# Optimization experiments

Hardware: AMD Instinct MI355X
Metric: run time of the kernel (lower is better)

## Reference

```python
import jax, jax.numpy as jnp
import numpy as np

E = 400000   # n_entity
R = 500      # n_relation
D = 128      # embed_dim
B = 2048     # batch of queries
K = 128      # sample_limit (refer neighbors per query)
GAMMA = 24.0
EPS = 2.0


def _xavier(key, fan_out, fan_in):
    lim = np.sqrt(6.0 / (fan_in + fan_out)).astype(np.float32)
    return jax.random.uniform(key, (fan_out, fan_in), minval=-lim, maxval=lim, dtype=jnp.float32)


def setup_inputs() -> dict:
    key = jax.random.key(0)
    ks = jax.random.split(key, 9)
    erange = (GAMMA + EPS) / D
    # tables with the appended zero padding row (as in forward's torch.cat)
    ent = jax.random.uniform(ks[0], (E + R + 1, D), minval=-erange, maxval=erange, dtype=jnp.float32)
    entity_embedding = jnp.concatenate([ent, jnp.zeros((1, D), jnp.float32)], axis=0)
    rel = jax.random.uniform(ks[1], (R + 1, D), minval=-erange, maxval=erange, dtype=jnp.float32)
    relation_embedding = jnp.concatenate([rel, jnp.zeros((1, D), jnp.float32)], axis=0)
    off = jax.random.uniform(ks[2], (R + 1, D), minval=0.0, maxval=erange, dtype=jnp.float32)
    offset_embedding = jnp.concatenate([off, jnp.zeros((1, D), jnp.float32)], axis=0)
    # ProjectionAggregating attention MLP params
    W1 = _xavier(ks[3], D, 2 * D)
    b1 = jnp.zeros((D,), jnp.float32)
    W2 = _xavier(ks[4], D, D)
    b2 = jnp.zeros((D,), jnp.float32)
    anchors = jax.random.randint(ks[5], (B,), 0, E)
    rel_0 = jax.random.randint(ks[6], (B,), 0, R)
    p1_target = jax.random.randint(ks[7], (B, K), 0, E)
    p1_rel = jax.random.randint(ks[8], (B, K), 0, R)
    return {
        'entity_embedding': entity_embedding,
        'relation_embedding': relation_embedding,
        'offset_embedding': offset_embedding,
        'W1': W1, 'b1': b1, 'W2': W2, 'b2': b2,
        'anchors': anchors, 'rel_0': rel_0,
        'p1_target': p1_target, 'p1_rel': p1_rel,
    }


def reference(entity_embedding, relation_embedding, offset_embedding,
              W1, b1, W2, b2, anchors, rel_0, p1_target, p1_rel):
    # ---- '1p' query path of IDN_Q2B_24.forward ----
    h_a = entity_embedding[anchors]            # [B, D]
    r_q = relation_embedding[rel_0]            # [B, D]
    query_emb = h_a + r_q                      # [B, D]
    offset_emb = offset_embedding[rel_0]       # [B, D]  (activation = Identity)
    h_t = entity_embedding[p1_target]          # [B, K, D]  refer_embs
    r_t = relation_embedding[p1_rel]           # [B, K, D]  refer_r
    # ProjectionAggregating (aggr='bias'): bias = refer - (start + refer_r)
    bias = h_t - (h_a[:, None, :] + r_t)       # [B, K, D]
    x = jnp.concatenate([r_t, jnp.broadcast_to(r_q[:, None, :], r_t.shape)], axis=-1)  # [B,K,2D]
    a1 = jax.nn.relu(jnp.einsum('bkf,df->bkd', x, W1) + b1)   # [B, K, D]
    attn = jnp.einsum('bkd,ed->bke', a1, W2) + b2             # [B, K, D]
    final_refer = jnp.sum(attn * bias, axis=-2)               # [B, D]
    final_query = query_emb + final_refer
    return final_query, offset_emb
```

## Files before the change

kernel.cpp:

```cpp
#include <hip/hip_runtime.h>

typedef __attribute__((ext_vector_type(8))) short short8;
typedef __attribute__((ext_vector_type(4))) float f32x4;

#define NRELROWS 502
#define NB 2048
#define DD 128
#define OUT_HALF (NB * DD)

__device__ __forceinline__ short f2bf(float x) {
    union { float f; unsigned u; } c; c.f = x;
    return (short)((c.u + 0x7FFFu + ((c.u >> 16) & 1u)) >> 16);
}

__global__ __launch_bounds__(256) void precompute_kernel(
    const float* __restrict__ rel, const float* __restrict__ W1,
    const float* __restrict__ b1, const float* __restrict__ W2,
    float* __restrict__ U, float* __restrict__ V,
    unsigned short* __restrict__ W2f)
{
    const int bid = blockIdx.x;
    const int tid = threadIdx.x;
    if (bid < 126) {
        __shared__ float srel[4][DD];
        const int r0 = bid << 2;
        for (int i = tid; i < 512; i += 256) {
            const int r = i >> 7, c = i & 127;
            const int rr = r0 + r;
            srel[r][c] = (rr < NRELROWS) ? rel[rr * DD + c] : 0.f;
        }
        __syncthreads();
        const int half = tid >> 7;
        const int d = tid & 127;
        const float* wrow = W1 + d * 256 + half * 128;
        float a0 = 0.f, a1 = 0.f, a2 = 0.f, a3 = 0.f;
#pragma unroll 8
        for (int f = 0; f < 128; f += 4) {
            const float4 wv = *(const float4*)(wrow + f);
            a0 += srel[0][f]*wv.x + srel[0][f+1]*wv.y + srel[0][f+2]*wv.z + srel[0][f+3]*wv.w;
            a1 += srel[1][f]*wv.x + srel[1][f+1]*wv.y + srel[1][f+2]*wv.z + srel[1][f+3]*wv.w;
            a2 += srel[2][f]*wv.x + srel[2][f+1]*wv.y + srel[2][f+2]*wv.z + srel[2][f+3]*wv.w;
            a3 += srel[3][f]*wv.x + srel[3][f+1]*wv.y + srel[3][f+2]*wv.z + srel[3][f+3]*wv.w;
        }
        float res[4] = {a0, a1, a2, a3};
        const float bb = half ? b1[d] : 0.f;
#pragma unroll
        for (int r = 0; r < 4; ++r) {
            if (r0 + r < NRELROWS) {
                if (half) V[(r0 + r) * DD + d] = res[r] + bb;
                else      U[(r0 + r) * DD + d] = res[r];
            }
        }
    } else {
        const int tile = bid - 126;
        const int kt = tile >> 3, nt = tile & 7;
#pragma unroll
        for (int e = 0; e < 2; ++e) {
            const int within = tid * 2 + e;
            const int l = within >> 3, i = within & 7;
            const int n = nt * 16 + (l & 15);
            const int f = kt * 32 + (l >> 4) * 8 + i;
            W2f[tile * 512 + within] = (unsigned short)f2bf(W2[n * 128 + f]);
        }
    }
}

__global__ __launch_bounds__(512, 4) void main_kernel(
    const float* __restrict__ ent, const float* __restrict__ rel,
    const float* __restrict__ off, const float* __restrict__ b2,
    const int* __restrict__ anchors, const int* __restrict__ rel0,
    const int* __restrict__ p1t, const int* __restrict__ p1r,
    const float* __restrict__ U, const float* __restrict__ V,
    const unsigned short* __restrict__ W2f, float* __restrict__ out)
{
    __shared__ float ht[128][DD];
    const int b = blockIdx.x;
    const int tid = threadIdx.x;
    const int w = tid >> 6;
    const int l = tid & 63;
    const int lg = l >> 4;
    const int l15 = l & 15;
    const int half = l >> 5;

    const int aidx = anchors[b];
    const int r0 = rel0[b];
    const int* p1t_b = p1t + (b << 7);
    const int* p1r_b = p1r + (b << 7);

    int rowi[8];
#pragma unroll
    for (int j = 0; j < 8; ++j)
        rowi[j] = p1t_b[(w << 4) + (j << 1) + half];
#pragma unroll
    for (int j = 0; j < 8; ++j) {
        const float* g = ent + (size_t)rowi[j] * DD + ((l & 31) << 2);
        float* lp = &ht[(w << 4) + (j << 1)][0];
        __builtin_amdgcn_global_load_lds(
            (const __attribute__((address_space(1))) unsigned int*)g,
            (__attribute__((address_space(3))) unsigned int*)lp, 16, 0, 0);
    }

    const int relA = p1r_b[(w << 4) + l15];

    f32x4 acc[8];
#pragma unroll
    for (int n = 0; n < 8; ++n) acc[n] = (f32x4)0.f;

    const float* Vrow = V + r0 * DD;
    const float* Urow0 = U + relA * DD;

#pragma unroll
    for (int kt = 0; kt < 4; ++kt) {
        const int f0 = kt * 32 + lg * 8;
        const float4 vv0 = *(const float4*)(Vrow + f0);
        const float4 vv1 = *(const float4*)(Vrow + f0 + 4);
        const float4 u0 = *(const float4*)(Urow0 + f0);
        const float4 u1 = *(const float4*)(Urow0 + f0 + 4);
        short8 af;
        af[0] = f2bf(fmaxf(u0.x + vv0.x, 0.f));
        af[1] = f2bf(fmaxf(u0.y + vv0.y, 0.f));
        af[2] = f2bf(fmaxf(u0.z + vv0.z, 0.f));
        af[3] = f2bf(fmaxf(u0.w + vv0.w, 0.f));
        af[4] = f2bf(fmaxf(u1.x + vv1.x, 0.f));
        af[5] = f2bf(fmaxf(u1.y + vv1.y, 0.f));
        af[6] = f2bf(fmaxf(u1.z + vv1.z, 0.f));
        af[7] = f2bf(fmaxf(u1.w + vv1.w, 0.f));
        const unsigned short* Wk = W2f + (kt << 3) * 512 + (l << 3);
#pragma unroll
        for (int nt = 0; nt < 8; ++nt) {
            const short8 bf = *(const short8*)(Wk + (nt << 9));
            acc[nt] = __builtin_amdgcn_mfma_f32_16x16x32_bf16(af, bf, acc[nt], 0, 0, 0);
        }
    }

    const int4 r4 = *(const int4*)(p1r_b + (w << 4) + (lg << 2));
    const int rr4[4] = {r4.x, r4.y, r4.z, r4.w};
    const float* arow = ent + (size_t)aidx * DD;

    asm volatile("s_waitcnt vmcnt(0)" ::: "memory");
    __builtin_amdgcn_sched_barrier(0);

    float ps[8];
#pragma unroll
    for (int nt = 0; nt < 8; ++nt) ps[nt] = 0.f;
#pragma unroll
    for (int nt = 0; nt < 8; ++nt) {
        const int d = (nt << 4) + l15;
        const float had = arow[d];
        const float b2d = b2[d];
#pragma unroll
        for (int r2 = 0; r2 < 4; ++r2) {
            const float at = acc[nt][r2] + b2d;
            const float hv = ht[(w << 4) + (lg << 2) + r2][d];
            const float rv = rel[rr4[r2] * DD + d];
            ps[nt] += at * (hv - had - rv);
        }
        ps[nt] += __shfl_xor(ps[nt], 16);
        ps[nt] += __shfl_xor(ps[nt], 32);
    }

    __syncthreads();
    float* red = &ht[0][0];
    if (lg == 0) {
#pragma unroll
        for (int nt = 0; nt < 8; ++nt)
            red[w * DD + (nt << 4) + l15] = ps[nt];
    }
    __syncthreads();
    if (tid < DD) {
        const int d = tid;
        float s = 0.f;
#pragma unroll
        for (int ww = 0; ww < 8; ++ww) s += red[ww * DD + d];
        out[(b << 7) + d] = arow[d] + rel[r0 * DD + d] + s;
        out[OUT_HALF + (b << 7) + d] = off[r0 * DD + d];
    }
}

extern "C" void kernel_launch(void* const* d_in, const int* in_sizes, int n_in,
                              void* d_out, int out_size, void* d_ws, size_t ws_size,
                              hipStream_t stream) {
    const float* ent  = (const float*)d_in[0];
    const float* rel  = (const float*)d_in[1];
    const float* off  = (const float*)d_in[2];
    const float* W1   = (const float*)d_in[3];
    const float* b1   = (const float*)d_in[4];
    const float* W2   = (const float*)d_in[5];
    const float* b2   = (const float*)d_in[6];
    const int* anchors = (const int*)d_in[7];
    const int* rel0    = (const int*)d_in[8];
    const int* p1t     = (const int*)d_in[9];
    const int* p1r     = (const int*)d_in[10];
    float* out = (float*)d_out;

    float* U = (float*)d_ws;
    float* V = U + NRELROWS * DD;
    unsigned short* W2f = (unsigned short*)(V + NRELROWS * DD);

    precompute_kernel<<<126 + 32, 256, 0, stream>>>(rel, W1, b1, W2, U, V, W2f);
    main_kernel<<<NB, 512, 0, stream>>>(ent, rel, off, b2, anchors, rel0,
                                        p1t, p1r, U, V, W2f, out);
}
```

Baseline: 61.10 us.

## Process eight queries per block with register-staged gather prefetch and LDS-resident W2

Each block now handles eight queries instead of one, looping over them. The bf16 W2 fragments are built once per block in LDS rather than by a separate precompute pass. The next query's entity rows are prefetched into registers while the current query's MFMA and reduction run, replacing the per-query async global-to-LDS load. This amortizes setup and overlaps the gather latency with compute, but it cuts the grid to 256 blocks and needs more LDS and registers per block, which may lower occupancy and parallelism.

Measured after the change: 66.94 us. 1.1x slower.

```diff
diff --git a/kernel.cpp b/kernel.cpp
--- a/kernel.cpp
+++ b/kernel.cpp
@@ -2,10 +2,13 @@
 
 typedef __attribute__((ext_vector_type(8))) short short8;
 typedef __attribute__((ext_vector_type(4))) float f32x4;
+typedef __attribute__((ext_vector_type(2))) float f32x2;
 
 #define NRELROWS 502
 #define NB 2048
 #define DD 128
+#define QPB 8
+#define NBLK (NB / QPB)
 #define OUT_HALF (NB * DD)
 
 __device__ __forceinline__ short f2bf(float x) {
@@ -15,165 +18,210 @@
 
 __global__ __launch_bounds__(256) void precompute_kernel(
     const float* __restrict__ rel, const float* __restrict__ W1,
-    const float* __restrict__ b1, const float* __restrict__ W2,
-    float* __restrict__ U, float* __restrict__ V,
-    unsigned short* __restrict__ W2f)
+    const float* __restrict__ b1,
+    float* __restrict__ U, float* __restrict__ V)
 {
     const int bid = blockIdx.x;
     const int tid = threadIdx.x;
-    if (bid < 126) {
-        __shared__ float srel[4][DD];
-        const int r0 = bid << 2;
-        for (int i = tid; i < 512; i += 256) {
-            const int r = i >> 7, c = i & 127;
-            const int rr = r0 + r;
-            srel[r][c] = (rr < NRELROWS) ? rel[rr * DD + c] : 0.f;
-        }
-        __syncthreads();
-        const int half = tid >> 7;
-        const int d = tid & 127;
-        const float* wrow = W1 + d * 256 + half * 128;
-        float a0 = 0.f, a1 = 0.f, a2 = 0.f, a3 = 0.f;
+    __shared__ float srel[4][DD];
+    const int r0 = bid << 2;
+    for (int i = tid; i < 512; i += 256) {
+        const int r = i >> 7, c = i & 127;
+        const int rr = r0 + r;
+        srel[r][c] = (rr < NRELROWS) ? rel[rr * DD + c] : 0.f;
+    }
+    __syncthreads();
+    const int half = tid >> 7;
+    const int d = tid & 127;
+    const float* wrow = W1 + d * 256 + half * 128;
+    float a0 = 0.f, a1 = 0.f, a2 = 0.f, a3 = 0.f;
 #pragma unroll 8
-        for (int f = 0; f < 128; f += 4) {
-            const float4 wv = *(const float4*)(wrow + f);
-            a0 += srel[0][f]*wv.x + srel[0][f+1]*wv.y + srel[0][f+2]*wv.z + srel[0][f+3]*wv.w;
-            a1 += srel[1][f]*wv.x + srel[1][f+1]*wv.y + srel[1][f+2]*wv.z + srel[1][f+3]*wv.w;
-            a2 += srel[2][f]*wv.x + srel[2][f+1]*wv.y + srel[2][f+2]*wv.z + srel[2][f+3]*wv.w;
-            a3 += srel[3][f]*wv.x + srel[3][f+1]*wv.y + srel[3][f+2]*wv.z + srel[3][f+3]*wv.w;
-        }
-        float res[4] = {a0, a1, a2, a3};
-        const float bb = half ? b1[d] : 0.f;
-#pragma unroll
-        for (int r = 0; r < 4; ++r) {
-            if (r0 + r < NRELROWS) {
-                if (half) V[(r0 + r) * DD + d] = res[r] + bb;
-                else      U[(r0 + r) * DD + d] = res[r];
-            }
-        }
-    } else {
-        const int tile = bid - 126;
-        const int kt = tile >> 3, nt = tile & 7;
-#pragma unroll
-        for (int e = 0; e < 2; ++e) {
-            const int within = tid * 2 + e;
-            const int l = within >> 3, i = within & 7;
-            const int n = nt * 16 + (l & 15);
-            const int f = kt * 32 + (l >> 4) * 8 + i;
-            W2f[tile * 512 + within] = (unsigned short)f2bf(W2[n * 128 + f]);
-        }
-    }
-}
-
-__global__ __launch_bounds__(512, 4) void main_kernel(
+    for (int f = 0; f < 128; f += 4) {
+        const float4 wv = *(const float4*)(wrow + f);
+        a0 += srel[0][f]*wv.x + srel[0][f+1]*wv.y + srel[0][f+2]*wv.z + srel[0][f+3]*wv.w;
+        a1 += srel[1][f]*wv.x + srel[1][f+1]*wv.y + srel[1][f+2]*wv.z + srel[1][f+3]*wv.w;
+        a2 += srel[2][f]*wv.x + srel[2][f+1]*wv.y + srel[2][f+2]*wv.z + srel[2][f+3]*wv.w;
+        a3 += srel[3][f]*wv.x + srel[3][f+1]*wv.y + srel[3][f+2]*wv.z + srel[3][f+3]*wv.w;
+    }
+    float res[4] = {a0, a1, a2, a3};
+    const float bb = half ? b1[d] : 0.f;
+#pragma unroll
+    for (int r = 0; r < 4; ++r) {
+        if (r0 + r < NRELROWS) {
+            if (half) V[(r0 + r) * DD + d] = res[r] + bb;
+            else      U[(r0 + r) * DD + d] = res[r];
+        }
+    }
+}
+
+__global__ __launch_bounds__(512) void main_kernel(
     const float* __restrict__ ent, const float* __restrict__ rel,
     const float* __restrict__ off, const float* __restrict__ b2,
+    const float* __restrict__ W2,
     const int* __restrict__ anchors, const int* __restrict__ rel0,
     const int* __restrict__ p1t, const int* __restrict__ p1r,
     const float* __restrict__ U, const float* __restrict__ V,
-    const unsigned short* __restrict__ W2f, float* __restrict__ out)
+    float* __restrict__ out)
 {
-    __shared__ float ht[128][DD];
-    const int b = blockIdx.x;
+    extern __shared__ float lds[];
+    float* ht = lds;
+    unsigned short* w2l = (unsigned short*)(lds + DD*DD);
+    float* red = (float*)(w2l + 32 * 512);
+
     const int tid = threadIdx.x;
     const int w = tid >> 6;
     const int l = tid & 63;
     const int lg = l >> 4;
     const int l15 = l & 15;
-    const int half = l >> 5;
-
-    const int aidx = anchors[b];
-    const int r0 = rel0[b];
-    const int* p1t_b = p1t + (b << 7);
-    const int* p1r_b = p1r + (b << 7);
-
-    int rowi[8];
-#pragma unroll
-    for (int j = 0; j < 8; ++j)
-        rowi[j] = p1t_b[(w << 4) + (j << 1) + half];
-#pragma unroll
-    for (int j = 0; j < 8; ++j) {
-        const float* g = ent + (size_t)rowi[j] * DD + ((l & 31) << 2);
-        float* lp = &ht[(w << 4) + (j << 1)][0];
-        __builtin_amdgcn_global_load_lds(
-            (const __attribute__((address_space(1))) unsigned int*)g,
-            (__attribute__((address_space(3))) unsigned int*)lp, 16, 0, 0);
-    }
-
-    const int relA = p1r_b[(w << 4) + l15];
-
-    f32x4 acc[8];
-#pragma unroll
-    for (int n = 0; n < 8; ++n) acc[n] = (f32x4)0.f;
-
-    const float* Vrow = V + r0 * DD;
-    const float* Urow0 = U + relA * DD;
-
-#pragma unroll
-    for (int kt = 0; kt < 4; ++kt) {
-        const int f0 = kt * 32 + lg * 8;
-        const float4 vv0 = *(const float4*)(Vrow + f0);
-        const float4 vv1 = *(const float4*)(Vrow + f0 + 4);
-        const float4 u0 = *(const float4*)(Urow0 + f0);
-        const float4 u1 = *(const float4*)(Urow0 + f0 + 4);
-        short8 af;
-        af[0] = f2bf(fmaxf(u0.x + vv0.x, 0.f));
-        af[1] = f2bf(fmaxf(u0.y + vv0.y, 0.f));
-        af[2] = f2bf(fmaxf(u0.z + vv0.z, 0.f));
-        af[3] = f2bf(fmaxf(u0.w + vv0.w, 0.f));
-        af[4] = f2bf(fmaxf(u1.x + vv1.x, 0.f));
-        af[5] = f2bf(fmaxf(u1.y + vv1.y, 0.f));
-        af[6] = f2bf(fmaxf(u1.z + vv1.z, 0.f));
-        af[7] = f2bf(fmaxf(u1.w + vv1.w, 0.f));
-        const unsigned short* Wk = W2f + (kt << 3) * 512 + (l << 3);
+    const int bq0 = blockIdx.x * QPB;
+
+    for (int i = tid; i < 32 * 512; i += 512) {
+        const int tile = i >> 9, within = i & 511;
+        const int kt = tile >> 3, nt = tile & 7;
+        const int ll = within >> 3, ii = within & 7;
+        const int n = nt * 16 + (ll & 15);
+        const int f = kt * 32 + (ll >> 4) * 8 + ii;
+        w2l[i] = (unsigned short)f2bf(W2[n * 128 + f]);
+    }
+    float b2v[8];
+#pragma unroll
+    for (int nt = 0; nt < 8; ++nt) b2v[nt] = b2[(nt << 4) + l15];
+
+    const int* p1t_0 = p1t + (bq0 << 7);
+    const int* p1r_0 = p1r + (bq0 << 7);
+    int relA = p1r_0[(w << 4) + l15];
+    int4 rr4 = *(const int4*)(p1r_0 + (w << 4) + (lg << 2));
+    int aidx = anchors[bq0];
+    int r0 = rel0[bq0];
+    f32x2 stg[16];
+    {
+        int4 ti[4];
+#pragma unroll
+        for (int j = 0; j < 4; ++j)
+            ti[j] = *(const int4*)(p1t_0 + (w << 4) + (j << 2));
+        int nrow[16] = {ti[0].x, ti[0].y, ti[0].z, ti[0].w,
+                        ti[1].x, ti[1].y, ti[1].z, ti[1].w,
+                        ti[2].x, ti[2].y, ti[2].z, ti[2].w,
+                        ti[3].x, ti[3].y, ti[3].z, ti[3].w};
+#pragma unroll
+        for (int r = 0; r < 16; ++r)
+            stg[r] = *(const f32x2*)(ent + (size_t)nrow[r] * DD + (l << 1));
+    }
+    asm volatile("s_waitcnt lgkmcnt(0)" ::: "memory");
+    __builtin_amdgcn_s_barrier();
+
+#pragma unroll 1
+    for (int q = 0; q < QPB; ++q) {
+        const int qg = bq0 + q;
+#pragma unroll
+        for (int r = 0; r < 16; ++r)
+            *(f32x2*)(ht + (size_t)((w << 4) + r) * DD + (l << 1)) = stg[r];
+
+        const int qn = (q + 1 < QPB) ? (q + 1) : q;
+        const int* p1t_n = p1t + ((bq0 + qn) << 7);
+        const int* p1r_n = p1r + ((bq0 + qn) << 7);
+        int4 ti[4];
+#pragma unroll
+        for (int j = 0; j < 4; ++j)
+            ti[j] = *(const int4*)(p1t_n + (w << 4) + (j << 2));
+        const int n_relA = p1r_n[(w << 4) + l15];
+        const int4 n_rr4 = *(const int4*)(p1r_n + (w << 4) + (lg << 2));
+        const int n_aidx = anchors[bq0 + qn];
+        const int n_r0 = rel0[bq0 + qn];
+
+        const float* Vrow = V + r0 * DD;
+        const float* Urow = U + relA * DD;
+        short8 af[4];
+#pragma unroll
+        for (int kt = 0; kt < 4; ++kt) {
+            const int f0 = kt * 32 + lg * 8;
+            const float4 vv0 = *(const float4*)(Vrow + f0);
+            const float4 vv1 = *(const float4*)(Vrow + f0 + 4);
+            const float4 u0 = *(const float4*)(Urow + f0);
+            const float4 u1 = *(const float4*)(Urow + f0 + 4);
+            af[kt][0] = f2bf(fmaxf(u0.x + vv0.x, 0.f));
+            af[kt][1] = f2bf(fmaxf(u0.y + vv0.y, 0.f));
+            af[kt][2] = f2bf(fmaxf(u0.z + vv0.z, 0.f));
+            af[kt][3] = f2bf(fmaxf(u0.w + vv0.w, 0.f));
+            af[kt][4] = f2bf(fmaxf(u1.x + vv1.x, 0.f));
+            af[kt][5] = f2bf(fmaxf(u1.y + vv1.y, 0.f));
+            af[kt][6] = f2bf(fmaxf(u1.z + vv1.z, 0.f));
+            af[kt][7] = f2bf(fmaxf(u1.w + vv1.w, 0.f));
+        }
+        const int rrk[4] = {rr4.x, rr4.y, rr4.z, rr4.w};
+        float rv[8][4];
+#pragma unroll
+        for (int r2 = 0; r2 < 4; ++r2) {
+            const float* rp = rel + rrk[r2] * DD + l15;
+#pragma unroll
+            for (int nt = 0; nt < 8; ++nt) rv[nt][r2] = rp[nt << 4];
+        }
+        const float* ar = ent + (size_t)aidx * DD + l15;
+        float hav[8];
+#pragma unroll
+        for (int nt = 0; nt < 8; ++nt) hav[nt] = ar[nt << 4];
+        const int d2 = tid & 127;
+        const float o_a = ent[(size_t)aidx * DD + d2];
+        const float o_r = rel[r0 * DD + d2];
+        const float o_o = off[r0 * DD + d2];
+        __builtin_amdgcn_sched_barrier(0);
+
+        {
+            int nrow[16] = {ti[0].x, ti[0].y, ti[0].z, ti[0].w,
+                            ti[1].x, ti[1].y, ti[1].z, ti[1].w,
+                            ti[2].x, ti[2].y, ti[2].z, ti[2].w,
+                            ti[3].x, ti[3].y, ti[3].z, ti[3].w};
+#pragma unroll
+            for (int r = 0; r < 16; ++r)
+                stg[r] = *(const f32x2*)(ent + (size_t)nrow[r] * DD + (l << 1));
+        }
+        __builtin_amdgcn_sched_barrier(0);
+
+        f32x4 acc[8];
+#pragma unroll
+        for (int nt = 0; nt < 8; ++nt) acc[nt] = (f32x4)0.f;
+#pragma unroll
+        for (int kt = 0; kt < 4; ++kt) {
+#pragma unroll
+            for (int nt = 0; nt < 8; ++nt) {
+                const short8 bf = *(const short8*)(w2l + ((kt << 3) + nt) * 512 + (l << 3));
+                acc[nt] = __builtin_amdgcn_mfma_f32_16x16x32_bf16(af[kt], bf, acc[nt], 0, 0, 0);
+            }
+        }
+
+        float psv[8];
 #pragma unroll
         for (int nt = 0; nt < 8; ++nt) {
-            const short8 bf = *(const short8*)(Wk + (nt << 9));
-            acc[nt] = __builtin_amdgcn_mfma_f32_16x16x32_bf16(af, bf, acc[nt], 0, 0, 0);
-        }
-    }
-
-    const int4 r4 = *(const int4*)(p1r_b + (w << 4) + (lg << 2));
-    const int rr4[4] = {r4.x, r4.y, r4.z, r4.w};
-    const float* arow = ent + (size_t)aidx * DD;
-
-    asm volatile("s_waitcnt vmcnt(0)" ::: "memory");
-    __builtin_amdgcn_sched_barrier(0);
-
-    float ps[8];
-#pragma unroll
-    for (int nt = 0; nt < 8; ++nt) ps[nt] = 0.f;
-#pragma unroll
-    for (int nt = 0; nt < 8; ++nt) {
-        const int d = (nt << 4) + l15;
-        const float had = arow[d];
-        const float b2d = b2[d];
-#pragma unroll
-        for (int r2 = 0; r2 < 4; ++r2) {
-            const float at = acc[nt][r2] + b2d;
-            const float hv = ht[(w << 4) + (lg << 2) + r2][d];
-            const float rv = rel[rr4[r2] * DD + d];
-            ps[nt] += at * (hv - had - rv);
-        }
-        ps[nt] += __shfl_xor(ps[nt], 16);
-        ps[nt] += __shfl_xor(ps[nt], 32);
-    }
-
-    __syncthreads();
-    float* red = &ht[0][0];
-    if (lg == 0) {
-#pragma unroll
-        for (int nt = 0; nt < 8; ++nt)
-            red[w * DD + (nt << 4) + l15] = ps[nt];
-    }
-    __syncthreads();
-    if (tid < DD) {
-        const int d = tid;
-        float s = 0.f;
-#pragma unroll
-        for (int ww = 0; ww < 8; ++ww) s += red[ww * DD + d];
-        out[(b << 7) + d] = arow[d] + rel[r0 * DD + d] + s;
-        out[OUT_HALF + (b << 7) + d] = off[r0 * DD + d];
+            const int d = (nt << 4) + l15;
+            float p = 0.f;
+#pragma unroll
+            for (int r2 = 0; r2 < 4; ++r2) {
+                const float at = acc[nt][r2] + b2v[nt];
+                const float hv = ht[(size_t)((w << 4) + (lg << 2) + r2) * DD + d];
+                p += at * (hv - hav[nt] - rv[nt][r2]);
+            }
+            p += __shfl_xor(p, 16);
+            p += __shfl_xor(p, 32);
+            psv[nt] = p;
+        }
+
+        if (lg == 0) {
+#pragma unroll
+            for (int nt = 0; nt < 8; ++nt)
+                red[w * DD + (nt << 4) + l15] = psv[nt];
+        }
+        asm volatile("s_waitcnt lgkmcnt(0)" ::: "memory");
+        __builtin_amdgcn_s_barrier();
+        if (tid < DD) {
+            float s = 0.f;
+#pragma unroll
+            for (int ww = 0; ww < 8; ++ww) s += red[ww * DD + tid];
+            out[(qg << 7) + tid] = o_a + o_r + s;
+            out[OUT_HALF + (qg << 7) + tid] = o_o;
+        }
+        __builtin_amdgcn_s_barrier();
+
+        relA = n_relA; rr4 = n_rr4; aidx = n_aidx; r0 = n_r0;
     }
 }
 
@@ -195,9 +243,13 @@
 
     float* U = (float*)d_ws;
     float* V = U + NRELROWS * DD;
-    unsigned short* W2f = (unsigned short*)(V + NRELROWS * DD);
-
-    precompute_kernel<<<126 + 32, 256, 0, stream>>>(rel, W1, b1, W2, U, V, W2f);
-    main_kernel<<<NB, 512, 0, stream>>>(ent, rel, off, b2, anchors, rel0,
-                                        p1t, p1r, U, V, W2f, out);
-}
+
+    const int lds_bytes = DD * DD * 4 + 32 * 512 * 2 + 8 * DD * 4;
+    hipFuncSetAttribute((const void*)main_kernel,
+                        hipFuncAttributeMaxDynamicSharedMemorySize, lds_bytes);
+
+    precompute_kernel<<<126, 256, 0, stream>>>(rel, W1, b1, U, V);
+    main_kernel<<<NBLK, 512, lds_bytes, stream>>>(ent, rel, off, b2, W2,
+                                                  anchors, rel0, p1t, p1r,
+                                                  U, V, out);
+}
```
